# Kernel optimization log

Measured on AMD Instinct MI355X. Metric: run time of the kernel, lower is better.

## Reference

```python
import jax, jax.numpy as jnp
import numpy as np

D_MODEL = 256
N_HEAD = 8


def quick_gelu(x):
    return x * jax.nn.sigmoid(1.702 * x)


def setup_inputs() -> dict:
    key = jax.random.key(0)
    ks = jax.random.split(key, 7)
    d = D_MODEL
    s = 0.02
    return {
        "x": jax.random.normal(ks[0], (2, 512, d), dtype=jnp.float32),
        "W_qkv": jax.random.normal(ks[1], (d, 3 * d), dtype=jnp.float32) * s,
        "b_qkv": jnp.zeros((3 * d,), dtype=jnp.float32),
        "W_fc": jax.random.normal(ks[2], (d, 4 * d), dtype=jnp.float32) * s,
        "b_fc": jnp.zeros((4 * d,), dtype=jnp.float32),
        "W_proj": jax.random.normal(ks[3], (4 * d, d), dtype=jnp.float32) * s,
        "b_proj": jnp.zeros((d,), dtype=jnp.float32),
    }


def attention_l1(x, W_qkv, b_qkv):
    bs, n_ctx, width = x.shape
    h = N_HEAD
    c = width // h
    scale = 1.0 / jnp.sqrt(jnp.asarray(c, x.dtype))
    qkv = (x @ W_qkv + b_qkv).reshape(bs, n_ctx, h, 3 * c)
    q, k, v = jnp.split(qkv, 3, axis=-1)  # each (b, t, h, c)
    qh = q.transpose(0, 2, 1, 3)  # (b, h, t, c)
    kh = k.transpose(0, 2, 1, 3)  # (b, h, s, c)
    vh = v.transpose(0, 2, 1, 3)  # (b, h, s, c)
    # L1 distance: sum_c |q - k| * scale  -> (b, h, t, s)
    dist = jnp.sum(jnp.abs(qh[:, :, :, None, :] - kh[:, :, None, :, :]), axis=-1) * scale
    weight = 1.0 / (0.001 + dist)
    idx = jnp.arange(n_ctx)
    weight = weight.at[:, :, idx, idx].set(0.0)
    wdtype = weight.dtype
    weight = jax.nn.softmax(weight.astype(jnp.float32), axis=-1).astype(wdtype)
    out = jnp.einsum('bhts,bhsc->bthc', weight, vh)
    return out.reshape(bs, n_ctx, width)


def reference(x, W_qkv, b_qkv, W_fc, b_fc, W_proj, b_proj):
    x = x + attention_l1(x, W_qkv, b_qkv)
    h = quick_gelu(x @ W_fc + b_fc)
    x = x + (h @ W_proj + b_proj)
    return x
```

## Files before the change

### kernel.cpp

```cpp
#include <hip/hip_runtime.h>
#include <hip/hip_bf16.h>

#define DM   256
#define NH   8
#define HC   32
#define SEQ  512
#define MTOT 1024

#define OFF_Q    0
#define OFF_K    262144
#define OFF_X1   524288
#define FP32_END 786432
#define BOFF_X1B    262144
#define BOFF_HB     524288
#define BOFF_VTB    1572864
#define BOFF_WQKVT  1835008
#define BOFF_WFCT   2031616
#define BOFF_WPROJT 2293760

typedef __attribute__((ext_vector_type(8))) __bf16 bf16x8;
typedef __attribute__((ext_vector_type(4))) __bf16 bf16x4;
typedef __attribute__((ext_vector_type(4))) float  f32x4;

__device__ __forceinline__ float qgelu(float x) {
    return x / (1.0f + __expf(-1.702f * x));
}

__global__ __launch_bounds__(256)
void trans_k(const float* __restrict__ Wqkv, const float* __restrict__ Wfc,
             const float* __restrict__ Wproj, __bf16* __restrict__ wsb)
{
    __shared__ float lt[64 * 65];
    const int bid = blockIdx.x, tid = threadIdx.x;
    const float* src; __bf16* dst; int K, N, tile;
    if (bid < 48)       { src = Wqkv;  dst = wsb + BOFF_WQKVT;  K = 256;  N = 768;  tile = bid; }
    else if (bid < 112) { src = Wfc;   dst = wsb + BOFF_WFCT;   K = 256;  N = 1024; tile = bid - 48; }
    else                { src = Wproj; dst = wsb + BOFF_WPROJT; K = 1024; N = 256;  tile = bid - 112; }
    const int nn = N >> 6;
    const int k0 = (tile / nn) * 64, n0 = (tile % nn) * 64;
    const int rr0 = tid >> 4, c4 = tid & 15;
    #pragma unroll
    for (int i = 0; i < 4; ++i) {
        const int rr = rr0 + i * 16;
        float4 v = *(const float4*)&src[(size_t)(k0 + rr) * N + n0 + c4 * 4];
        lt[rr * 65 + c4 * 4 + 0] = v.x; lt[rr * 65 + c4 * 4 + 1] = v.y;
        lt[rr * 65 + c4 * 4 + 2] = v.z; lt[rr * 65 + c4 * 4 + 3] = v.w;
    }
    __syncthreads();
    #pragma unroll
    for (int i = 0; i < 4; ++i) {
        const int rr = rr0 + i * 16;
        bf16x4 b;
        b.x = (__bf16)lt[(c4 * 4 + 0) * 65 + rr];
        b.y = (__bf16)lt[(c4 * 4 + 1) * 65 + rr];
        b.z = (__bf16)lt[(c4 * 4 + 2) * 65 + rr];
        b.w = (__bf16)lt[(c4 * 4 + 3) * 65 + rr];
        *(bf16x4*)&dst[(size_t)(n0 + rr) * K + k0 + c4 * 4] = b;
    }
}

__global__ __launch_bounds__(256)
void qkv_k(const float* __restrict__ x, const __bf16* __restrict__ Bt,
           const float* __restrict__ bias, float* __restrict__ ws,
           __bf16* __restrict__ vtb)
{
    const int lane = threadIdx.x & 63, wv = threadIdx.x >> 6;
    const int widx = blockIdx.x * 4 + wv;
    const int m0 = (widx & 63) * 16, n0 = (widx >> 6) * 16;
    const int r = lane & 15, q = lane >> 4;

    const float*  ap = x  + (size_t)(m0 + r) * DM + q * 8;
    const __bf16* bp = Bt + (size_t)(n0 + r) * DM + q * 8;

    f32x4 acc = {0.f, 0.f, 0.f, 0.f};
    #pragma unroll
    for (int kt = 0; kt < DM; kt += 32) {
        float4 a0 = *(const float4*)(ap + kt);
        float4 a1 = *(const float4*)(ap + kt + 4);
        bf16x8 af;
        af[0] = (__bf16)a0.x; af[1] = (__bf16)a0.y; af[2] = (__bf16)a0.z; af[3] = (__bf16)a0.w;
        af[4] = (__bf16)a1.x; af[5] = (__bf16)a1.y; af[6] = (__bf16)a1.z; af[7] = (__bf16)a1.w;
        bf16x8 bf = *(const bf16x8*)(bp + kt);
        acc = __builtin_amdgcn_mfma_f32_16x16x32_bf16(af, bf, acc, 0, 0, 0);
    }

    const int n = n0 + r;
    const float bn = bias[n];
    const int h = n / 96, jj = n % 96;
    #pragma unroll
    for (int i = 0; i < 4; ++i) {
        const int m = m0 + q * 4 + i;
        const float v = acc[i] + bn;
        const int b = m >> 9, t = m & 511;
        const int bh = b * NH + h;
        if (jj < 32)      ws[OFF_Q + ((size_t)(bh * SEQ + t)) * HC + jj]        = v;
        else if (jj < 64) ws[OFF_K + ((size_t)(bh * SEQ + t)) * HC + (jj - 32)] = v;
        else              vtb[((size_t)(bh * HC + (jj - 64))) * SEQ + t] = (__bf16)v;
    }
}

#define QT 16
#define PSTRIDE 514

__global__ __launch_bounds__(512, 4)
void attn_k(const float* __restrict__ wq, const float* __restrict__ wk,
            const __bf16* __restrict__ vtb, const float* __restrict__ xin,
            float* __restrict__ x1, __bf16* __restrict__ x1b)
{
    __shared__ float  qtile[QT * 32];
    __shared__ __bf16 pmat[QT * PSTRIDE];
    __shared__ float  psum[QT * 8];
    __shared__ float  pinv[QT];

    const int tid  = threadIdx.x;
    const int lane = tid & 63;
    const int wv   = tid >> 6;
    const int sg   = tid;
    const int bh   = blockIdx.x >> 5;
    const int qbase = (blockIdx.x & 31) * QT;
    const float scale = 0.17677669529663687f;

    const float* krow = wk + ((size_t)(bh * SEQ + sg)) * HC;
    float kr[32];
    #pragma unroll
    for (int j = 0; j < 8; ++j) {
        float4 k4 = *(const float4*)&krow[j * 4];
        kr[j*4+0] = k4.x; kr[j*4+1] = k4.y; kr[j*4+2] = k4.z; kr[j*4+3] = k4.w;
    }
    if (tid < QT * 32 / 4) {
        *(float4*)&qtile[tid * 4] =
            *(const float4*)&wq[((size_t)(bh * SEQ + qbase)) * HC + tid * 4];
    }
    __syncthreads();

    #pragma unroll 4
    for (int t = 0; t < QT; ++t) {
        float d = 0.f;
        #pragma unroll
        for (int j = 0; j < 8; ++j) {
            float4 q4 = *(const float4*)&qtile[t * 32 + j * 4];
            d += fabsf(kr[j*4+0] - q4.x) + fabsf(kr[j*4+1] - q4.y)
               + fabsf(kr[j*4+2] - q4.z) + fabsf(kr[j*4+3] - q4.w);
        }
        float w = 1.0f / (0.001f + d * scale);
        if (sg == qbase + t) w = 0.0f;
        float p = __expf(w);
        float se = p;
        #pragma unroll
        for (int off = 32; off >= 1; off >>= 1) se += __shfl_xor(se, off, 64);
        pmat[t * PSTRIDE + sg] = (__bf16)p;
        if (lane == 0) psum[t * 8 + wv] = se;
    }
    __syncthreads();

    if (tid < QT) {
        float s = 0.f;
        #pragma unroll
        for (int j = 0; j < 8; ++j) s += psum[tid * 8 + j];
        pinv[tid] = 1.0f / s;
    }
    __syncthreads();

    if (wv < 2) {
        const int r = lane & 15, q = lane >> 4;
        const __bf16* bp  = vtb + ((size_t)(bh * HC + wv * 16 + r)) * SEQ + q * 8;
        const __bf16* apm = &pmat[r * PSTRIDE + q * 8];
        f32x4 acc = {0.f, 0.f, 0.f, 0.f};
        #pragma unroll
        for (int kt = 0; kt < SEQ; kt += 32) {
            bf16x8 af = *(const bf16x8*)(apm + kt);
            bf16x8 bf = *(const bf16x8*)(bp + kt);
            acc = __builtin_amdgcn_mfma_f32_16x16x32_bf16(af, bf, acc, 0, 0, 0);
        }
        const int b = bh >> 3, hh = bh & 7;
        const int c = wv * 16 + r;
        #pragma unroll
        for (int i = 0; i < 4; ++i) {
            const int tl = q * 4 + i;
            const int t  = qbase + tl;
            const float v = acc[i] * pinv[tl];
            const int idx = ((b * SEQ + t) * DM) + hh * HC + c;
            const float res = xin[idx] + v;
            x1[idx]  = res;
            x1b[idx] = (__bf16)res;
        }
    }
}

__global__ __launch_bounds__(256)
void fc_k(const __bf16* __restrict__ A, const __bf16* __restrict__ Bt,
          const float* __restrict__ bias, __bf16* __restrict__ Ob)
{
    const int lane = threadIdx.x & 63, wv = threadIdx.x >> 6;
    const int widx = blockIdx.x * 4 + wv;
    const int m0 = (widx & 63) * 16, n0 = (widx >> 6) * 16;
    const int r = lane & 15, q = lane >> 4;

    const __bf16* ap = A  + (size_t)(m0 + r) * DM + q * 8;
    const __bf16* bp = Bt + (size_t)(n0 + r) * DM + q * 8;

    f32x4 acc = {0.f, 0.f, 0.f, 0.f};
    #pragma unroll
    for (int kt = 0; kt < DM; kt += 32) {
        bf16x8 af = *(const bf16x8*)(ap + kt);
        bf16x8 bf = *(const bf16x8*)(bp + kt);
        acc = __builtin_amdgcn_mfma_f32_16x16x32_bf16(af, bf, acc, 0, 0, 0);
    }

    const int n = n0 + r;
    const float bn = bias[n];
    #pragma unroll
    for (int i = 0; i < 4; ++i) {
        const int m = m0 + q * 4 + i;
        Ob[(size_t)m * 1024 + n] = (__bf16)qgelu(acc[i] + bn);
    }
}

__global__ __launch_bounds__(256)
void proj_k(const __bf16* __restrict__ H, const __bf16* __restrict__ Bt,
            const float* __restrict__ bias, const float* __restrict__ X1,
            float* __restrict__ out)
{
    __shared__ f32x4 ared[4][64];
    const int lane = threadIdx.x & 63, wv = threadIdx.x >> 6;
    const int tile = blockIdx.x;
    const int m0 = (tile & 63) * 16, n0 = (tile >> 6) * 16;
    const int r = lane & 15, q = lane >> 4;

    const __bf16* ap = H  + (size_t)(m0 + r) * 1024 + wv * 256 + q * 8;
    const __bf16* bp = Bt + (size_t)(n0 + r) * 1024 + wv * 256 + q * 8;

    f32x4 acc = {0.f, 0.f, 0.f, 0.f};
    #pragma unroll
    for (int kk = 0; kk < 8; ++kk) {
        bf16x8 af = *(const bf16x8*)(ap + kk * 32);
        bf16x8 bf = *(const bf16x8*)(bp + kk * 32);
        acc = __builtin_amdgcn_mfma_f32_16x16x32_bf16(af, bf, acc, 0, 0, 0);
    }
    ared[wv][lane] = acc;
    __syncthreads();

    if (wv == 0) {
        f32x4 a0 = ared[0][lane], a1 = ared[1][lane];
        f32x4 a2 = ared[2][lane], a3 = ared[3][lane];
        const int n = n0 + r;
        const float bn = bias[n];
        #pragma unroll
        for (int i = 0; i < 4; ++i) {
            const int m = m0 + q * 4 + i;
            const float v = a0[i] + a1[i] + a2[i] + a3[i] + bn;
            out[(size_t)m * DM + n] = X1[(size_t)m * DM + n] + v;
        }
    }
}

extern "C" void kernel_launch(void* const* d_in, const int* in_sizes, int n_in,
                              void* d_out, int out_size, void* d_ws, size_t ws_size,
                              hipStream_t stream)
{
    (void)in_sizes; (void)n_in; (void)out_size; (void)ws_size;
    const float* x     = (const float*)d_in[0];
    const float* Wqkv  = (const float*)d_in[1];
    const float* bqkv  = (const float*)d_in[2];
    const float* Wfc   = (const float*)d_in[3];
    const float* bfc   = (const float*)d_in[4];
    const float* Wproj = (const float*)d_in[5];
    const float* bproj = (const float*)d_in[6];
    float* out = (float*)d_out;
    float* ws  = (float*)d_ws;
    __bf16* wsb = (__bf16*)(ws + FP32_END);

    trans_k<<<176, 256, 0, stream>>>(Wqkv, Wfc, Wproj, wsb);

    qkv_k<<<768, 256, 0, stream>>>(x, wsb + BOFF_WQKVT, bqkv, ws, wsb + BOFF_VTB);

    attn_k<<<512, 512, 0, stream>>>(ws + OFF_Q, ws + OFF_K, wsb + BOFF_VTB,
                                    x, ws + OFF_X1, wsb + BOFF_X1B);

    fc_k<<<1024, 256, 0, stream>>>(wsb + BOFF_X1B, wsb + BOFF_WFCT, bfc,
                                   wsb + BOFF_HB);

    proj_k<<<1024, 256, 0, stream>>>(wsb + BOFF_HB, wsb + BOFF_WPROJT, bproj,
                                     ws + OFF_X1, out);
}
```

Measured before the change: 117.6 us.

## Fuse weight transposes into QKV launch and use fp16 packed L1 distance

```diff
diff --git a/kernel.cpp b/kernel.cpp
--- a/kernel.cpp
+++ b/kernel.cpp
@@ -1,5 +1,6 @@
 #include <hip/hip_runtime.h>
 #include <hip/hip_bf16.h>
+#include <hip/hip_fp16.h>
 
 #define DM   256
 #define NH   8
@@ -7,16 +8,13 @@
 #define SEQ  512
 #define MTOT 1024
 
-#define OFF_Q    0
-#define OFF_K    262144
-#define OFF_X1   524288
-#define FP32_END 786432
-#define BOFF_X1B    262144
-#define BOFF_HB     524288
-#define BOFF_VTB    1572864
-#define BOFF_WQKVT  1835008
-#define BOFF_WFCT   2031616
-#define BOFF_WPROJT 2293760
+#define B_X1   0
+#define B_QH   (1u<<20)
+#define B_KH   0x180000u
+#define B_VT   0x200000u
+#define B_HB   0x280000u
+#define B_WFCT 0x480000u
+#define B_WPJT 0x500000u
 
 typedef __attribute__((ext_vector_type(8))) __bf16 bf16x8;
 typedef __attribute__((ext_vector_type(4))) __bf16 bf16x4;
@@ -27,49 +25,185 @@
 }
 
 __global__ __launch_bounds__(256)
-void trans_k(const float* __restrict__ Wqkv, const float* __restrict__ Wfc,
-             const float* __restrict__ Wproj, __bf16* __restrict__ wsb)
+void qkv_k(const float* __restrict__ x, const float* __restrict__ W,
+           const float* __restrict__ bias,
+           const float* __restrict__ Wfc, const float* __restrict__ Wproj,
+           char* __restrict__ wsb)
 {
     __shared__ float lt[64 * 65];
     const int bid = blockIdx.x, tid = threadIdx.x;
-    const float* src; __bf16* dst; int K, N, tile;
-    if (bid < 48)       { src = Wqkv;  dst = wsb + BOFF_WQKVT;  K = 256;  N = 768;  tile = bid; }
-    else if (bid < 112) { src = Wfc;   dst = wsb + BOFF_WFCT;   K = 256;  N = 1024; tile = bid - 48; }
-    else                { src = Wproj; dst = wsb + BOFF_WPROJT; K = 1024; N = 256;  tile = bid - 112; }
-    const int nn = N >> 6;
-    const int k0 = (tile / nn) * 64, n0 = (tile % nn) * 64;
-    const int rr0 = tid >> 4, c4 = tid & 15;
+
+    if (bid >= 768) {
+        const int tt = bid - 768;
+        const float* src; __bf16* dst; int K, N, tile;
+        if (tt < 64) { src = Wfc;   dst = (__bf16*)(wsb + B_WFCT); K = 256;  N = 1024; tile = tt; }
+        else         { src = Wproj; dst = (__bf16*)(wsb + B_WPJT); K = 1024; N = 256;  tile = tt - 64; }
+        const int nn = N >> 6;
+        const int k0 = (tile / nn) * 64, n0 = (tile % nn) * 64;
+        const int rr0 = tid >> 4, c4 = tid & 15;
+        #pragma unroll
+        for (int i = 0; i < 4; ++i) {
+            const int rr = rr0 + i * 16;
+            float4 v = *(const float4*)&src[(size_t)(k0 + rr) * N + n0 + c4 * 4];
+            lt[rr * 65 + c4 * 4 + 0] = v.x; lt[rr * 65 + c4 * 4 + 1] = v.y;
+            lt[rr * 65 + c4 * 4 + 2] = v.z; lt[rr * 65 + c4 * 4 + 3] = v.w;
+        }
+        __syncthreads();
+        #pragma unroll
+        for (int i = 0; i < 4; ++i) {
+            const int rr = rr0 + i * 16;
+            bf16x4 b;
+            b.x = (__bf16)lt[(c4 * 4 + 0) * 65 + rr];
+            b.y = (__bf16)lt[(c4 * 4 + 1) * 65 + rr];
+            b.z = (__bf16)lt[(c4 * 4 + 2) * 65 + rr];
+            b.w = (__bf16)lt[(c4 * 4 + 3) * 65 + rr];
+            *(bf16x4*)&dst[(size_t)(n0 + rr) * K + k0 + c4 * 4] = b;
+        }
+        return;
+    }
+
+    const int lane = tid & 63, wv = tid >> 6;
+    const int widx = bid * 4 + wv;
+    const int m0 = (widx & 63) * 16, n0 = (widx >> 6) * 16;
+    const int r = lane & 15, q = lane >> 4;
+
+    const float* ap = x + (size_t)(m0 + r) * DM + q * 8;
+    const float* bp = W + (size_t)(q * 8) * 768 + n0 + r;
+
+    f32x4 acc = {0.f, 0.f, 0.f, 0.f};
+    #pragma unroll
+    for (int kt = 0; kt < DM; kt += 32) {
+        float4 a0 = *(const float4*)(ap + kt);
+        float4 a1 = *(const float4*)(ap + kt + 4);
+        bf16x8 af;
+        af[0] = (__bf16)a0.x; af[1] = (__bf16)a0.y; af[2] = (__bf16)a0.z; af[3] = (__bf16)a0.w;
+        af[4] = (__bf16)a1.x; af[5] = (__bf16)a1.y; af[6] = (__bf16)a1.z; af[7] = (__bf16)a1.w;
+        bf16x8 bf;
+        #pragma unroll
+        for (int j = 0; j < 8; ++j)
+            bf[j] = (__bf16)bp[(size_t)(kt + j) * 768];
+        acc = __builtin_amdgcn_mfma_f32_16x16x32_bf16(af, bf, acc, 0, 0, 0);
+    }
+
+    __half*  qh  = (__half*)(wsb + B_QH);
+    __half*  kh  = (__half*)(wsb + B_KH);
+    __bf16*  vtb = (__bf16*)(wsb + B_VT);
+    const int n = n0 + r;
+    const float bn = bias[n];
+    const int h = n / 96, jj = n % 96;
     #pragma unroll
     for (int i = 0; i < 4; ++i) {
-        const int rr = rr0 + i * 16;
-        float4 v = *(const float4*)&src[(size_t)(k0 + rr) * N + n0 + c4 * 4];
-        lt[rr * 65 + c4 * 4 + 0] = v.x; lt[rr * 65 + c4 * 4 + 1] = v.y;
-        lt[rr * 65 + c4 * 4 + 2] = v.z; lt[rr * 65 + c4 * 4 + 3] = v.w;
-    }
-    __syncthreads();
-    #pragma unroll
-    for (int i = 0; i < 4; ++i) {
-        const int rr = rr0 + i * 16;
-        bf16x4 b;
-        b.x = (__bf16)lt[(c4 * 4 + 0) * 65 + rr];
-        b.y = (__bf16)lt[(c4 * 4 + 1) * 65 + rr];
-        b.z = (__bf16)lt[(c4 * 4 + 2) * 65 + rr];
-        b.w = (__bf16)lt[(c4 * 4 + 3) * 65 + rr];
-        *(bf16x4*)&dst[(size_t)(n0 + rr) * K + k0 + c4 * 4] = b;
+        const int m = m0 + q * 4 + i;
+        const float v = acc[i] + bn;
+        const int b = m >> 9, t = m & 511;
+        const int bh = b * NH + h;
+        if (jj < 32)      qh[((size_t)(bh * SEQ + t)) * HC + jj]        = (__half)v;
+        else if (jj < 64) kh[((size_t)(bh * SEQ + t)) * HC + (jj - 32)] = (__half)v;
+        else              vtb[((size_t)(bh * HC + (jj - 64))) * SEQ + t] = (__bf16)v;
+    }
+}
+
+#define QT 16
+#define PSTRIDE 514
+
+__global__ __launch_bounds__(512, 4)
+void attn_k(const char* __restrict__ wsb, const float* __restrict__ xin,
+            float* __restrict__ x1)
+{
+    __shared__ __half2 qtile[QT * 16];
+    __shared__ __bf16  pmat[QT * PSTRIDE];
+    __shared__ float   psum[QT * 8];
+    __shared__ float   pinv[QT];
+
+    const __half*  qhg = (const __half*)(wsb + B_QH);
+    const __half*  khg = (const __half*)(wsb + B_KH);
+    const __bf16*  vtb = (const __bf16*)(wsb + B_VT);
+
+    const int tid  = threadIdx.x;
+    const int lane = tid & 63;
+    const int wv   = tid >> 6;
+    const int sg   = tid;
+    const int bh   = blockIdx.x >> 5;
+    const int qbase = (blockIdx.x & 31) * QT;
+    const float scale = 0.17677669529663687f;
+
+    const __half2* kp = (const __half2*)(khg + ((size_t)(bh * SEQ + sg)) * HC);
+    __half2 kr[16];
+    #pragma unroll
+    for (int j = 0; j < 16; ++j) kr[j] = kp[j];
+
+    if (tid < 256) {
+        const int t = tid >> 4, j = tid & 15;
+        qtile[t * 16 + j] =
+            *(const __half2*)(qhg + ((size_t)(bh * SEQ + qbase + t)) * HC + j * 2);
+    }
+    __syncthreads();
+
+    #pragma unroll 4
+    for (int t = 0; t < QT; ++t) {
+        __half2 acc2 = __floats2half2_rn(0.f, 0.f);
+        #pragma unroll
+        for (int j = 0; j < 16; ++j) {
+            __half2 dif = __hsub2(kr[j], qtile[t * 16 + j]);
+            unsigned u = (*(unsigned*)&dif) & 0x7FFF7FFFu;
+            acc2 = __hadd2(acc2, *(__half2*)&u);
+        }
+        const float d = __low2float(acc2) + __high2float(acc2);
+        float w = 1.0f / (0.001f + d * scale);
+        if (sg == qbase + t) w = 0.0f;
+        float p = __expf(w);
+        float se = p;
+        #pragma unroll
+        for (int off = 32; off >= 1; off >>= 1) se += __shfl_xor(se, off, 64);
+        pmat[t * PSTRIDE + sg] = (__bf16)p;
+        if (lane == 0) psum[t * 8 + wv] = se;
+    }
+    __syncthreads();
+
+    if (tid < QT) {
+        float s = 0.f;
+        #pragma unroll
+        for (int j = 0; j < 8; ++j) s += psum[tid * 8 + j];
+        pinv[tid] = 1.0f / s;
+    }
+    __syncthreads();
+
+    if (wv < 2) {
+        const int r = lane & 15, q = lane >> 4;
+        const __bf16* bp  = vtb + ((size_t)(bh * HC + wv * 16 + r)) * SEQ + q * 8;
+        const __bf16* apm = &pmat[r * PSTRIDE + q * 8];
+        f32x4 acc = {0.f, 0.f, 0.f, 0.f};
+        #pragma unroll
+        for (int kt = 0; kt < SEQ; kt += 32) {
+            bf16x8 af = *(const bf16x8*)(apm + kt);
+            bf16x8 bf = *(const bf16x8*)(bp + kt);
+            acc = __builtin_amdgcn_mfma_f32_16x16x32_bf16(af, bf, acc, 0, 0, 0);
+        }
+        const int b = bh >> 3, hh = bh & 7;
+        const int c = wv * 16 + r;
+        #pragma unroll
+        for (int i = 0; i < 4; ++i) {
+            const int tl = q * 4 + i;
+            const int t  = qbase + tl;
+            const float v = acc[i] * pinv[tl];
+            const int idx = ((b * SEQ + t) * DM) + hh * HC + c;
+            x1[idx] = xin[idx] + v;
+        }
     }
 }
 
 __global__ __launch_bounds__(256)
-void qkv_k(const float* __restrict__ x, const __bf16* __restrict__ Bt,
-           const float* __restrict__ bias, float* __restrict__ ws,
-           __bf16* __restrict__ vtb)
-{
+void fc_k(const float* __restrict__ X1, const char* __restrict__ wsb,
+          const float* __restrict__ bias)
+{
+    const __bf16* Bt = (const __bf16*)(wsb + B_WFCT);
+    __bf16* Ob = (__bf16*)(wsb + B_HB);
     const int lane = threadIdx.x & 63, wv = threadIdx.x >> 6;
     const int widx = blockIdx.x * 4 + wv;
     const int m0 = (widx & 63) * 16, n0 = (widx >> 6) * 16;
     const int r = lane & 15, q = lane >> 4;
 
-    const float*  ap = x  + (size_t)(m0 + r) * DM + q * 8;
+    const float*  ap = X1 + (size_t)(m0 + r) * DM + q * 8;
     const __bf16* bp = Bt + (size_t)(n0 + r) * DM + q * 8;
 
     f32x4 acc = {0.f, 0.f, 0.f, 0.f};
@@ -86,129 +220,6 @@
 
     const int n = n0 + r;
     const float bn = bias[n];
-    const int h = n / 96, jj = n % 96;
-    #pragma unroll
-    for (int i = 0; i < 4; ++i) {
-        const int m = m0 + q * 4 + i;
-        const float v = acc[i] + bn;
-        const int b = m >> 9, t = m & 511;
-        const int bh = b * NH + h;
-        if (jj < 32)      ws[OFF_Q + ((size_t)(bh * SEQ + t)) * HC + jj]        = v;
-        else if (jj < 64) ws[OFF_K + ((size_t)(bh * SEQ + t)) * HC + (jj - 32)] = v;
-        else              vtb[((size_t)(bh * HC + (jj - 64))) * SEQ + t] = (__bf16)v;
-    }
-}
-
-#define QT 16
-#define PSTRIDE 514
-
-__global__ __launch_bounds__(512, 4)
-void attn_k(const float* __restrict__ wq, const float* __restrict__ wk,
-            const __bf16* __restrict__ vtb, const float* __restrict__ xin,
-            float* __restrict__ x1, __bf16* __restrict__ x1b)
-{
-    __shared__ float  qtile[QT * 32];
-    __shared__ __bf16 pmat[QT * PSTRIDE];
-    __shared__ float  psum[QT * 8];
-    __shared__ float  pinv[QT];
-
-    const int tid  = threadIdx.x;
-    const int lane = tid & 63;
-    const int wv   = tid >> 6;
-    const int sg   = tid;
-    const int bh   = blockIdx.x >> 5;
-    const int qbase = (blockIdx.x & 31) * QT;
-    const float scale = 0.17677669529663687f;
-
-    const float* krow = wk + ((size_t)(bh * SEQ + sg)) * HC;
-    float kr[32];
-    #pragma unroll
-    for (int j = 0; j < 8; ++j) {
-        float4 k4 = *(const float4*)&krow[j * 4];
-        kr[j*4+0] = k4.x; kr[j*4+1] = k4.y; kr[j*4+2] = k4.z; kr[j*4+3] = k4.w;
-    }
-    if (tid < QT * 32 / 4) {
-        *(float4*)&qtile[tid * 4] =
-            *(const float4*)&wq[((size_t)(bh * SEQ + qbase)) * HC + tid * 4];
-    }
-    __syncthreads();
-
-    #pragma unroll 4
-    for (int t = 0; t < QT; ++t) {
-        float d = 0.f;
-        #pragma unroll
-        for (int j = 0; j < 8; ++j) {
-            float4 q4 = *(const float4*)&qtile[t * 32 + j * 4];
-            d += fabsf(kr[j*4+0] - q4.x) + fabsf(kr[j*4+1] - q4.y)
-               + fabsf(kr[j*4+2] - q4.z) + fabsf(kr[j*4+3] - q4.w);
-        }
-        float w = 1.0f / (0.001f + d * scale);
-        if (sg == qbase + t) w = 0.0f;
-        float p = __expf(w);
-        float se = p;
-        #pragma unroll
-        for (int off = 32; off >= 1; off >>= 1) se += __shfl_xor(se, off, 64);
-        pmat[t * PSTRIDE + sg] = (__bf16)p;
-        if (lane == 0) psum[t * 8 + wv] = se;
-    }
-    __syncthreads();
-
-    if (tid < QT) {
-        float s = 0.f;
-        #pragma unroll
-        for (int j = 0; j < 8; ++j) s += psum[tid * 8 + j];
-        pinv[tid] = 1.0f / s;
-    }
-    __syncthreads();
-
-    if (wv < 2) {
-        const int r = lane & 15, q = lane >> 4;
-        const __bf16* bp  = vtb + ((size_t)(bh * HC + wv * 16 + r)) * SEQ + q * 8;
-        const __bf16* apm = &pmat[r * PSTRIDE + q * 8];
-        f32x4 acc = {0.f, 0.f, 0.f, 0.f};
-        #pragma unroll
-        for (int kt = 0; kt < SEQ; kt += 32) {
-            bf16x8 af = *(const bf16x8*)(apm + kt);
-            bf16x8 bf = *(const bf16x8*)(bp + kt);
-            acc = __builtin_amdgcn_mfma_f32_16x16x32_bf16(af, bf, acc, 0, 0, 0);
-        }
-        const int b = bh >> 3, hh = bh & 7;
-        const int c = wv * 16 + r;
-        #pragma unroll
-        for (int i = 0; i < 4; ++i) {
-            const int tl = q * 4 + i;
-            const int t  = qbase + tl;
-            const float v = acc[i] * pinv[tl];
-            const int idx = ((b * SEQ + t) * DM) + hh * HC + c;
-            const float res = xin[idx] + v;
-            x1[idx]  = res;
-            x1b[idx] = (__bf16)res;
-        }
-    }
-}
-
-__global__ __launch_bounds__(256)
-void fc_k(const __bf16* __restrict__ A, const __bf16* __restrict__ Bt,
-          const float* __restrict__ bias, __bf16* __restrict__ Ob)
-{
-    const int lane = threadIdx.x & 63, wv = threadIdx.x >> 6;
-    const int widx = blockIdx.x * 4 + wv;
-    const int m0 = (widx & 63) * 16, n0 = (widx >> 6) * 16;
-    const int r = lane & 15, q = lane >> 4;
-
-    const __bf16* ap = A  + (size_t)(m0 + r) * DM + q * 8;
-    const __bf16* bp = Bt + (size_t)(n0 + r) * DM + q * 8;
-
-    f32x4 acc = {0.f, 0.f, 0.f, 0.f};
-    #pragma unroll
-    for (int kt = 0; kt < DM; kt += 32) {
-        bf16x8 af = *(const bf16x8*)(ap + kt);
-        bf16x8 bf = *(const bf16x8*)(bp + kt);
-        acc = __builtin_amdgcn_mfma_f32_16x16x32_bf16(af, bf, acc, 0, 0, 0);
-    }
-
-    const int n = n0 + r;
-    const float bn = bias[n];
     #pragma unroll
     for (int i = 0; i < 4; ++i) {
         const int m = m0 + q * 4 + i;
@@ -217,11 +228,12 @@
 }
 
 __global__ __launch_bounds__(256)
-void proj_k(const __bf16* __restrict__ H, const __bf16* __restrict__ Bt,
-            const float* __restrict__ bias, const float* __restrict__ X1,
-            float* __restrict__ out)
+void proj_k(const char* __restrict__ wsb, const float* __restrict__ bias,
+            const float* __restrict__ X1, float* __restrict__ out)
 {
     __shared__ f32x4 ared[4][64];
+    const __bf16* H  = (const __bf16*)(wsb + B_HB);
+    const __bf16* Bt = (const __bf16*)(wsb + B_WPJT);
     const int lane = threadIdx.x & 63, wv = threadIdx.x >> 6;
     const int tile = blockIdx.x;
     const int m0 = (tile & 63) * 16, n0 = (tile >> 6) * 16;
@@ -267,19 +279,14 @@
     const float* Wproj = (const float*)d_in[5];
     const float* bproj = (const float*)d_in[6];
     float* out = (float*)d_out;
-    float* ws  = (float*)d_ws;
-    __bf16* wsb = (__bf16*)(ws + FP32_END);
-
-    trans_k<<<176, 256, 0, stream>>>(Wqkv, Wfc, Wproj, wsb);
-
-    qkv_k<<<768, 256, 0, stream>>>(x, wsb + BOFF_WQKVT, bqkv, ws, wsb + BOFF_VTB);
-
-    attn_k<<<512, 512, 0, stream>>>(ws + OFF_Q, ws + OFF_K, wsb + BOFF_VTB,
-                                    x, ws + OFF_X1, wsb + BOFF_X1B);
-
-    fc_k<<<1024, 256, 0, stream>>>(wsb + BOFF_X1B, wsb + BOFF_WFCT, bfc,
-                                   wsb + BOFF_HB);
-
-    proj_k<<<1024, 256, 0, stream>>>(wsb + BOFF_HB, wsb + BOFF_WPROJT, bproj,
-                                     ws + OFF_X1, out);
-}
+    char*  wsb = (char*)d_ws;
+    float* x1  = (float*)(wsb + B_X1);
+
+    qkv_k<<<896, 256, 0, stream>>>(x, Wqkv, bqkv, Wfc, Wproj, wsb);
+
+    attn_k<<<512, 512, 0, stream>>>(wsb, x, x1);
+
+    fc_k<<<1024, 256, 0, stream>>>(x1, wsb, bfc);
+
+    proj_k<<<1024, 256, 0, stream>>>(wsb, bproj, x1, out);
+}
```

New measurement: 114.5 us. -2.7%, faster.
